# Performance work log

Hardware: AMD Instinct MI355X
Metric: run time of the kernel (lower is better)

Reference implementation:

```python
import jax, jax.numpy as jnp
import numpy as np

B, S, D, H, W1, G = 2, 4096, 768, 12, 256, 8  # W1 = one-sided window (attention_window // 2)
HD = D // H
NC = S // W1  # number of query chunks of size W1
NEG = -1e9


def setup_inputs():
    key = jax.random.key(0)
    ks = jax.random.split(key, 9)
    def w(k):
        return jax.random.normal(k, (D, D), jnp.float32) * 0.02
    zb = jnp.zeros((D,), jnp.float32)
    # mask: >0 global, 0 local, <0 masked. First G tokens are global.
    mask = jnp.zeros((B, 1, 1, S), jnp.int32).at[:, :, :, :G].set(1)
    return {
        "hidden_states": jax.random.normal(ks[0], (B, S, D), jnp.float32),
        "attention_mask": mask,
        "Wq": w(ks[1]), "bq": zb,
        "Wk": w(ks[2]), "bk": zb,
        "Wv": w(ks[3]), "bv": zb,
        "Wqg": w(ks[4]), "bqg": zb,
        "Wkg": w(ks[5]), "bkg": zb,
        "Wvg": w(ks[6]), "bvg": zb,
        "Wo": w(ks[7]), "bo": zb,
        "n_global": G,
    }


def reference(hidden_states, attention_mask, Wq, bq, Wk, bk, Wv, bv,
              Wqg, bqg, Wkg, bkg, Wvg, bvg, Wo, bo, n_global):
    g = n_global
    mask = attention_mask.reshape(B, S)
    key_neg = mask < 0  # masked-out positions
    scale = 1.0 / np.sqrt(HD)

    def heads(x):  # [B,S,D] -> [B,H,S,HD]
        return x.reshape(B, S, H, HD).transpose(0, 2, 1, 3)

    q = heads(hidden_states @ Wq + bq) * scale
    k = heads(hidden_states @ Wk + bk)
    v = heads(hidden_states @ Wv + bv)

    # ---- sliding-window (banded) scores via 3-chunk gather ----
    idx = jnp.arange(NC)[:, None] * W1 + jnp.arange(3 * W1)[None, :]  # [NC,3W] into padded seq
    k_ch = jnp.pad(k, ((0, 0), (0, 0), (W1, W1), (0, 0)))[:, :, idx]  # [B,H,NC,3W,HD]
    q_ch = q.reshape(B, H, NC, W1, HD)
    band = jnp.einsum('bhcqd,bhckd->bhcqk', q_ch, k_ch)  # [B,H,NC,W,3W]

    qi = jnp.arange(W1)
    kj = jnp.arange(3 * W1)
    band_ok = jnp.abs(kj[None, :] - W1 - qi[:, None]) <= W1        # [W,3W] |j-i|<=w
    j_abs = idx - W1                                               # absolute key index
    in_range = (j_abs >= 0) & (j_abs < S)                          # [NC,3W]
    neg_ch = jnp.pad(key_neg, ((0, 0), (W1, W1)))[:, idx]          # [B,NC,3W]
    valid = (band_ok[None, None, None]
             & in_range[None, None, :, None, :]
             & (~neg_ch)[:, None, :, None, :])                     # [B,1,NC,W,3W]
    band = jnp.where(valid, band, NEG)

    # ---- scores of every query against the global keys (regular k proj) ----
    glob = jnp.einsum('bhsd,bhgd->bhsg', q, k[:, :, :g])           # [B,H,S,G]
    glob = jnp.where(key_neg[:, None, None, :g], NEG, glob)

    scores = jnp.concatenate([glob.reshape(B, H, NC, W1, g), band], axis=-1)
    probs = jax.nn.softmax(scores, axis=-1)
    probs = jnp.where(key_neg.reshape(B, 1, NC, W1, 1), 0.0, probs)  # zero masked query rows

    v_ch = jnp.pad(v, ((0, 0), (0, 0), (W1, W1), (0, 0)))[:, :, idx]
    out = jnp.einsum('bhcqk,bhckd->bhcqd', probs[..., g:], v_ch)
    out = out + jnp.einsum('bhcqg,bhgd->bhcqd', probs[..., :g], v[:, :, :g])
    out = out.reshape(B, H, S, HD)

    # ---- global tokens: full attention with dedicated global projections ----
    qg = heads(hidden_states @ Wqg + bqg)[:, :, :g] * scale        # [B,H,G,HD]
    kg = heads(hidden_states @ Wkg + bkg)
    vg = heads(hidden_states @ Wvg + bvg)
    gs = jnp.einsum('bhgd,bhsd->bhgs', qg, kg)                     # [B,H,G,S]
    gs = jnp.where(key_neg[:, None, None, :], NEG, gs)
    gp = jax.nn.softmax(gs, axis=-1)
    og = jnp.einsum('bhgs,bhsd->bhgd', gp, vg)
    out = out.at[:, :, :g].set(og)

    merged = out.transpose(0, 2, 1, 3).reshape(B, S, D)
    return merged @ Wo + bo  # outer output projection
```

## Files before the change

kernel.cpp:

```cpp
#include <hip/hip_runtime.h>

#define BB 2
#define SS 4096
#define DD 768
#define HH 12
#define HDD 64
#define W1C 256
#define NCC 16
#define GG 8

typedef unsigned short u16;
typedef __attribute__((ext_vector_type(4))) unsigned short u16x4;
typedef __attribute__((ext_vector_type(8))) unsigned short u16x8;
typedef __attribute__((ext_vector_type(8))) short s16x8;
typedef __attribute__((ext_vector_type(4))) float f32x4;

__device__ __forceinline__ float b2f(u16 u) {
  union { unsigned int i; float f; } v;
  v.i = ((unsigned int)u) << 16;
  return v.f;
}
__device__ __forceinline__ u16 f2b(float f) {
  union { float f; unsigned int i; } v;
  v.f = f;
  unsigned int r = v.i + 0x7FFFu + ((v.i >> 16) & 1u);
  return (u16)(r >> 16);
}
__device__ __forceinline__ float fexp2(float x) {
#if __has_builtin(__builtin_amdgcn_exp2f)
  return __builtin_amdgcn_exp2f(x);
#else
  return exp2f(x);
#endif
}
__device__ __forceinline__ unsigned pk_bf16(float lo, float hi) {
  unsigned r;
  asm("v_cvt_pk_bf16_f32 %0, %1, %2" : "=v"(r) : "v"(lo), "v"(hi));
  return r;
}
__device__ __forceinline__ void load_lds16(const void* g, void* l) {
  __builtin_amdgcn_global_load_lds(
      (const __attribute__((address_space(1))) unsigned int*)g,
      (__attribute__((address_space(3))) unsigned int*)l, 16, 0, 0);
}

#define QSCALE 0.18033688011112042f

__global__ __launch_bounds__(256) void cvt_f32_bf16(
    const float* __restrict__ in, u16* __restrict__ out, int n8) {
  int i = blockIdx.x * 256 + threadIdx.x;
  if (i >= n8) return;
  const float4* p = (const float4*)(in + (size_t)i * 8);
  float4 a = p[0], b = p[1];
  u16x8 o;
  o[0] = f2b(a.x); o[1] = f2b(a.y); o[2] = f2b(a.z); o[3] = f2b(a.w);
  o[4] = f2b(b.x); o[5] = f2b(b.y); o[6] = f2b(b.z); o[7] = f2b(b.w);
  *(u16x8*)(out + (size_t)i * 8) = o;
}

struct WtArgs { const float* W[6]; };

__global__ __launch_bounds__(256) void transpose_wt(WtArgs wa,
                                                    u16* __restrict__ WT) {
  __shared__ float T[64][65];
  const int mat = blockIdx.z;
  const int k0 = blockIdx.y * 64;
  const int n0 = blockIdx.x * 64;
  const float* __restrict__ W = wa.W[mat];
  const int t = threadIdx.x;
#pragma unroll
  for (int i = 0; i < 4; i++) {
    int idx4 = t + i * 256;
    int r = idx4 >> 4, c4 = idx4 & 15;
    float4 v = *(const float4*)(W + (size_t)(k0 + r) * 768 + n0 + c4 * 4);
    T[r][c4 * 4 + 0] = v.x; T[r][c4 * 4 + 1] = v.y;
    T[r][c4 * 4 + 2] = v.z; T[r][c4 * 4 + 3] = v.w;
  }
  __syncthreads();
#pragma unroll
  for (int i = 0; i < 2; i++) {
    int ci = t + i * 256;
    int nl = ci >> 3, k8 = ci & 7;
    u16x8 o;
#pragma unroll
    for (int jj = 0; jj < 8; jj++) o[jj] = f2b(T[k8 * 8 + jj][nl]);
    *(u16x8*)(WT + ((size_t)mat * 768 + n0 + nl) * 768 + k0 + k8 * 8) = o;
  }
}

struct BiasArgs { const float* bias[5]; };

template <int MODE>
__global__ __launch_bounds__(256) void gemm_bf16(
    const u16* __restrict__ A, const u16* __restrict__ WT, BiasArgs ba,
    u16* __restrict__ outb, float* __restrict__ outf) {
  __shared__ __align__(16) u16 As[128 * 32];
  __shared__ __align__(16) u16 Bs[128 * 32];
  const int tid = threadIdx.x;
  const int w = tid >> 6, l = tid & 63;
  const int m0 = blockIdx.y * 128;
  const int wsel = (MODE == 0) ? ((int)blockIdx.x / 6) : 0;
  const int n0 =
      (MODE == 0) ? (((int)blockIdx.x % 6) * 128) : ((int)blockIdx.x * 128);
  const int nw0 = (int)blockIdx.x * 128;
  const float* __restrict__ bias = ba.bias[wsel];
  const int wm = w >> 1, wn = w & 1;
  const int srow = l >> 2;
  const int skc = (l & 3) * 8;

  f32x4 acc[4][4];
#pragma unroll
  for (int i = 0; i < 4; i++)
#pragma unroll
    for (int j = 0; j < 4; j++) acc[i][j] = (f32x4){0.f, 0.f, 0.f, 0.f};

  for (int k0 = 0; k0 < 768; k0 += 32) {
    __syncthreads();
#pragma unroll
    for (int i = 0; i < 2; i++) {
      const int ci = i * 4 + w;
      load_lds16(A + (size_t)(m0 + ci * 16 + srow) * 768 + k0 + skc,
                 (char*)As + ci * 1024);
    }
#pragma unroll
    for (int i = 0; i < 2; i++) {
      const int ci = i * 4 + w;
      load_lds16(WT + (size_t)(nw0 + ci * 16 + srow) * 768 + k0 + skc,
                 (char*)Bs + ci * 1024);
    }
    asm volatile("s_waitcnt vmcnt(0)" ::: "memory");
    __syncthreads();
    s16x8 af[4], bf[4];
#pragma unroll
    for (int mi = 0; mi < 4; mi++)
      af[mi] = *(const s16x8*)(As + (wm * 64 + mi * 16 + (l & 15)) * 32 +
                               (l >> 4) * 8);
#pragma unroll
    for (int nj = 0; nj < 4; nj++)
      bf[nj] = *(const s16x8*)(Bs + (wn * 64 + nj * 16 + (l & 15)) * 32 +
                               (l >> 4) * 8);
#pragma unroll
    for (int mi = 0; mi < 4; mi++)
#pragma unroll
      for (int nj = 0; nj < 4; nj++)
        acc[mi][nj] = __builtin_amdgcn_mfma_f32_16x16x32_bf16(
            af[mi], bf[nj], acc[mi][nj], 0, 0, 0);
  }

  const int rbase = (l >> 4) * 4;
  const int cl = l & 15;
  if (MODE == 0) {
    const float scale = (wsel == 0) ? QSCALE : 1.0f;
    u16* outw = outb + (size_t)wsel * ((size_t)BB * HH * SS * HDD);
#pragma unroll
    for (int nj = 0; nj < 4; nj++) {
      const int c = n0 + wn * 64 + nj * 16 + cl;
      const float bv = bias[c];
      const int h = c >> 6, hd = c & 63;
#pragma unroll
      for (int mi = 0; mi < 4; mi++) {
#pragma unroll
        for (int r = 0; r < 4; r++) {
          const int m = m0 + wm * 64 + mi * 16 + rbase + r;
          const int b = m >> 12, s = m & 4095;
          outw[((size_t)(b * HH + h) * SS + s) * HDD + hd] =
              f2b((acc[mi][nj][r] + bv) * scale);
        }
      }
    }
  } else {
#pragma unroll
    for (int nj = 0; nj < 4; nj++) {
      const int c = n0 + wn * 64 + nj * 16 + cl;
      const float bv = bias[c];
#pragma unroll
      for (int mi = 0; mi < 4; mi++) {
#pragma unroll
        for (int r = 0; r < 4; r++) {
          const int m = m0 + wm * 64 + mi * 16 + rbase + r;
          outf[(size_t)m * 768 + c] = acc[mi][nj][r] + bv;
        }
      }
    }
  }
}

__global__ __launch_bounds__(256) void qg_proj(
    const float* __restrict__ hs, const float* __restrict__ Wqg,
    const float* __restrict__ bqg, u16* __restrict__ QG) {
  __shared__ float hsL[8][768];
  const int bh = blockIdx.x;
  const int b = bh / HH, h = bh % HH;
  const int t = threadIdx.x;
#pragma unroll
  for (int i = 0; i < 6; i++) {
    int idx = t + i * 256;
    int row = idx / 192, c4 = idx % 192;
    *(float4*)&hsL[row][c4 * 4] =
        *(const float4*)(hs + ((size_t)b * SS + row) * DD + c4 * 4);
  }
  __syncthreads();
#pragma unroll
  for (int rep = 0; rep < 2; rep++) {
    int qi = rep * 4 + (t >> 6);
    int d = t & 63, n = h * 64 + d;
    float acc = bqg[n];
    for (int k = 0; k < DD; k++)
      acc = fmaf(hsL[qi][k], Wqg[(size_t)k * DD + n], acc);
    QG[((size_t)bh * 16 + qi) * 64 + d] = f2b(acc * QSCALE);
  }
#pragma unroll
  for (int i = 0; i < 2; i++) {
    int idx = t + i * 256;
    int row = 8 + (idx >> 6), d = idx & 63;
    QG[((size_t)bh * 16 + row) * 64 + d] = 0;
  }
}

template <int GLOBAL>
__global__ __launch_bounds__(256) void attn_mfma(
    const u16* __restrict__ Q, const u16* __restrict__ K,
    const u16* __restrict__ V, const int* __restrict__ amask,
    u16* __restrict__ ATT, float* __restrict__ Pnum,
    float* __restrict__ Pden) {
  extern __shared__ __align__(16) char smem[];
  const int tid = threadIdx.x;
  const int w = tid >> 6, lane = tid & 63;
  const int lq = lane & 15, g = lane >> 4;
  const int h = blockIdx.y, b = blockIdx.z;
  const int bh = b * HH + h;
  const size_t bhs = (size_t)bh * SS;
  const int q0 = GLOBAL ? 0 : (int)blockIdx.x * 64;
  const int split = GLOBAL ? (int)blockIdx.x : 0;

  char* Kl;
  char* VT;
  if constexpr (GLOBAL) {
    Kl = smem + w * 16384;
    VT = Kl + 8192;
  } else {
    Kl = smem;
    VT = smem + 8192;
  }

  s16x8 qf[2];
  {
    const u16* qp = GLOBAL ? (Q + ((size_t)bh * 16 + lq) * 64)
                           : (Q + (bhs + q0 + w * 16 + lq) * 64);
    qf[0] = *(const s16x8*)(qp + g * 8);
    qf[1] = *(const s16x8*)(qp + 32 + g * 8);
  }

  f32x4 oacc[4];
#pragma unroll
  for (int i = 0; i < 4; i++) oacc[i] = (f32x4){0.f, 0.f, 0.f, 0.f};
  float denom = 0.f;

  const int NT = GLOBAL ? 2 : 10;
  for (int kt = 0; kt < NT; kt++) {
    int j0, klimit;
    bool bandfree;
    if constexpr (GLOBAL) {
      j0 = split * 512 + (w * 2 + kt) * 64;
      bandfree = true;
      klimit = 64;
    } else {
      if (kt < 9) { j0 = q0 - 256 + kt * 64; bandfree = false; klimit = 64; }
      else        { j0 = 0;                  bandfree = true;  klimit = 8; }
    }

    int jm = j0 + lane;
    int mv = ((unsigned)jm < (unsigned)SS) ? amask[b * SS + jm] : -1;
    bool okk = (mv >= 0) && (lane < klimit);
    unsigned long long vm = __ballot(okk);

    if constexpr (GLOBAL) {
      asm volatile("s_waitcnt lgkmcnt(0)" ::: "memory");
      const u16* Ks = K + bhs * 64 + (size_t)j0 * 64;
#pragma unroll
      for (int i = 0; i < 8; i++) {
        int ci = i * 64 + lane;
        int row = ci >> 3, cc = ci & 7, cs = cc ^ (row & 7);
        load_lds16(Ks + row * 64 + cs * 8, Kl + i * 1024);
      }
      const u16* Vs = V + bhs * 64 + (size_t)j0 * 64;
#pragma unroll
      for (int p = 0; p < 8; p++) {
        u16x8 vv = *(const u16x8*)(Vs + (size_t)lane * 64 + p * 8);
#pragma unroll
        for (int e = 0; e < 8; e++)
          *(u16*)(VT + (p * 8 + e) * 128 + ((lane * 2) ^ (e << 4))) = vv[e];
      }
      asm volatile("s_waitcnt vmcnt(0) lgkmcnt(0)" ::: "memory");
    } else {
      __syncthreads();
      if (j0 >= 0 && j0 + 64 <= SS) {
        const u16* Ks = K + bhs * 64 + (size_t)j0 * 64;
#pragma unroll
        for (int i = 0; i < 2; i++) {
          int ci = (i * 4 + w) * 64 + lane;
          int row = ci >> 3, cc = ci & 7, cs = cc ^ (row & 7);
          load_lds16(Ks + row * 64 + cs * 8, Kl + (i * 4 + w) * 1024);
        }
      } else {
#pragma unroll
        for (int i = 0; i < 2; i++) {
          int ci = (i * 4 + w) * 64 + lane;
          int row = ci >> 3, cc = ci & 7, cs = cc ^ (row & 7);
          int jj = j0 + row;
          u16x8 val;
#pragma unroll
          for (int e = 0; e < 8; e++) val[e] = 0;
          if ((unsigned)jj < (unsigned)SS)
            val = *(const u16x8*)(K + (bhs + jj) * 64 + cs * 8);
          *(u16x8*)(Kl + ci * 16) = val;
        }
      }
#pragma unroll
      for (int p = 0; p < 2; p++) {
        int d0 = p * 32 + w * 8;
        int jj = j0 + lane;
        u16x8 vv;
#pragma unroll
        for (int e = 0; e < 8; e++) vv[e] = 0;
        if ((unsigned)jj < (unsigned)SS)
          vv = *(const u16x8*)(V + (bhs + jj) * 64 + d0);
#pragma unroll
        for (int e = 0; e < 8; e++)
          *(u16*)(VT + (d0 + e) * 128 + ((lane * 2) ^ (e << 4))) = vv[e];
      }
      asm volatile("s_waitcnt vmcnt(0)" ::: "memory");
      __syncthreads();
    }

    f32x4 sc[4];
#pragma unroll
    for (int i = 0; i < 4; i++) sc[i] = (f32x4){0.f, 0.f, 0.f, 0.f};
#pragma unroll
    for (int s = 0; s < 2; s++) {
#pragma unroll
      for (int ks = 0; ks < 4; ks++) {
        s16x8 kf = *(const s16x8*)(Kl + (ks * 16 + lq) * 128 +
                                   (((s * 4 + g) ^ (lq & 7)) << 4));
        sc[ks] = __builtin_amdgcn_mfma_f32_16x16x32_bf16(kf, qf[s], sc[ks],
                                                          0, 0, 0);
      }
    }

    {
      const unsigned mlo = (unsigned)vm, mhi = (unsigned)(vm >> 32);
      const int q_abs = q0 + w * 16 + lq;
      bool allin = bandfree;
      if constexpr (!GLOBAL) {
        const int qw = q0 + w * 16;
        allin = bandfree || (j0 >= qw - 241 && j0 <= qw + 193);
      }
      const bool fast = (vm == ~0ull) && allin;
      const int ddq = j0 + g * 4 - q_abs;
      const int gsh = g * 4;
      if (fast) {
#pragma unroll
        for (int ks = 0; ks < 4; ks++)
#pragma unroll
          for (int r = 0; r < 4; r++) {
            float p = fexp2(sc[ks][r]);
            sc[ks][r] = p;
            denom += p;
          }
      } else {
#pragma unroll
        for (int ks = 0; ks < 4; ks++)
#pragma unroll
          for (int r = 0; r < 4; r++) {
            float e = fexp2(sc[ks][r]);
            unsigned bit =
                ((ks < 2 ? mlo : mhi) >> (gsh + ((ks & 1) * 16 + r))) & 1u;
            bool ok = bit && (allin ||
                              (unsigned)(ddq + ks * 16 + r + 256) <= 512u);
            float p = ok ? e : 0.f;
            sc[ks][r] = p;
            denom += p;
          }
      }
    }

#pragma unroll
    for (int s = 0; s < 2; s++) {
      const int srcA = lq + ((g & 1) << 5);
      const bool hiSel = g >= 2;
      float L[4], H[4];
#pragma unroll
      for (int r = 0; r < 4; r++) {
        float a0 = __shfl(sc[2 * s][r], srcA);
        float a1 = __shfl(sc[2 * s + 1][r], srcA);
        L[r] = hiSel ? a1 : a0;
        float b0 = __shfl(sc[2 * s][r], srcA + 16);
        float b1 = __shfl(sc[2 * s + 1][r], srcA + 16);
        H[r] = hiSel ? b1 : b0;
      }
      union { unsigned u[4]; s16x8 v; } pf;
      pf.u[0] = pk_bf16(L[0], L[1]);
      pf.u[1] = pk_bf16(L[2], L[3]);
      pf.u[2] = pk_bf16(H[0], H[1]);
      pf.u[3] = pk_bf16(H[2], H[3]);
#pragma unroll
      for (int dblk = 0; dblk < 4; dblk++) {
        s16x8 vf = *(const s16x8*)(VT + (dblk * 16 + lq) * 128 +
                                   (((s * 4 + g) ^ (lq & 7)) << 4));
        oacc[dblk] = __builtin_amdgcn_mfma_f32_16x16x32_bf16(vf, pf.v,
                                                              oacc[dblk],
                                                              0, 0, 0);
      }
    }
  }

  denom += __shfl_xor(denom, 16);
  denom += __shfl_xor(denom, 32);
  if constexpr (!GLOBAL) {
    const int q_abs = q0 + w * 16 + lq;
    const float rowscale = (amask[b * SS + q_abs] >= 0) ? (1.f / denom) : 0.f;
    u16* orow = ATT + ((size_t)b * SS + q_abs) * DD + h * 64;
#pragma unroll
    for (int dblk = 0; dblk < 4; dblk++) {
      u16x4 o;
#pragma unroll
      for (int r = 0; r < 4; r++) o[r] = f2b(oacc[dblk][r] * rowscale);
      *(u16x4*)(orow + dblk * 16 + g * 4) = o;
    }
  } else {
    const int pidx = split * 4 + w;
    float* np = Pnum + ((size_t)bh * 32 + pidx) * 1024;
#pragma unroll
    for (int dblk = 0; dblk < 4; dblk++)
#pragma unroll
      for (int r = 0; r < 4; r++)
        np[(dblk * 16 + g * 4 + r) * 16 + lq] = oacc[dblk][r];
    Pden[((size_t)bh * 32 + pidx) * 16 + lq] = denom;
  }
}

__global__ __launch_bounds__(512) void gmerge(const float* __restrict__ Pnum,
                                              const float* __restrict__ Pden,
                                              u16* __restrict__ ATT) {
  const int bh = blockIdx.x;
  const int b = bh / HH, h = bh % HH;
  const int t = threadIdx.x;
  const int q = t >> 6, d = t & 63;
  float num = 0.f, den = 0.f;
#pragma unroll 4
  for (int p = 0; p < 32; p++) {
    num += Pnum[((size_t)bh * 32 + p) * 1024 + d * 16 + q];
    den += Pden[((size_t)bh * 32 + p) * 16 + q];
  }
  ATT[((size_t)b * SS + q) * DD + h * 64 + d] = f2b(num / den);
}

extern "C" void kernel_launch(void* const* d_in, const int* in_sizes, int n_in,
                              void* d_out, int out_size, void* d_ws,
                              size_t ws_size, hipStream_t stream) {
  const float* hs = (const float*)d_in[0];
  const int* amask = (const int*)d_in[1];
  const float* Wq = (const float*)d_in[2];
  const float* bq = (const float*)d_in[3];
  const float* Wk = (const float*)d_in[4];
  const float* bk = (const float*)d_in[5];
  const float* Wv = (const float*)d_in[6];
  const float* bv = (const float*)d_in[7];
  const float* Wqg = (const float*)d_in[8];
  const float* bqg = (const float*)d_in[9];
  const float* Wkg = (const float*)d_in[10];
  const float* bkg = (const float*)d_in[11];
  const float* Wvg = (const float*)d_in[12];
  const float* bvg = (const float*)d_in[13];
  const float* Wo = (const float*)d_in[14];
  const float* bo = (const float*)d_in[15];
  float* out = (float*)d_out;

  char* ws = (char*)d_ws;
  const size_t QSZB = (size_t)BB * HH * SS * HDD * 2;
  u16* Qb = (u16*)(ws + 0);
  u16* Kb = (u16*)(ws + QSZB);
  u16* Vb = (u16*)(ws + 2 * QSZB);
  u16* KGb = (u16*)(ws + 3 * QSZB);
  u16* VGb = (u16*)(ws + 4 * QSZB);
  u16* Ab = (u16*)(ws + 5 * QSZB);
  u16* WTb = (u16*)(ws + 6 * QSZB);
  u16* ATTb = (u16*)(ws + 6 * QSZB + 7077888);
  u16* QGb = (u16*)(ws + 7 * QSZB + 7077888);
  float* Pnum = (float*)(ws + 7 * QSZB + 7077888 + 49152);
  float* Pden = (float*)(ws + 7 * QSZB + 7077888 + 49152 + 3145728);

  hipLaunchKernelGGL(cvt_f32_bf16, dim3(3072), dim3(256), 0, stream, hs, Ab,
                     (int)((size_t)BB * SS * DD / 8));

  WtArgs wa;
  wa.W[0] = Wq; wa.W[1] = Wk; wa.W[2] = Wv;
  wa.W[3] = Wkg; wa.W[4] = Wvg; wa.W[5] = Wo;
  hipLaunchKernelGGL(transpose_wt, dim3(12, 12, 6), dim3(256), 0, stream, wa,
                     WTb);

  BiasArgs b0;
  b0.bias[0] = bq; b0.bias[1] = bk; b0.bias[2] = bv;
  b0.bias[3] = bkg; b0.bias[4] = bvg;
  hipLaunchKernelGGL((gemm_bf16<0>), dim3(30, 64), dim3(256), 0, stream, Ab,
                     WTb, b0, Qb, (float*)nullptr);

  hipLaunchKernelGGL(qg_proj, dim3(24), dim3(256), 0, stream, hs, Wqg, bqg,
                     QGb);

  hipLaunchKernelGGL((attn_mfma<1>), dim3(8, HH, BB), dim3(256), 65536,
                     stream, QGb, KGb, VGb, amask, (u16*)nullptr, Pnum, Pden);

  hipLaunchKernelGGL((attn_mfma<0>), dim3(64, HH, BB), dim3(256), 16384,
                     stream, Qb, Kb, Vb, amask, ATTb, (float*)nullptr,
                     (float*)nullptr);

  hipLaunchKernelGGL(gmerge, dim3(24), dim3(512), 0, stream, Pnum, Pden, ATTb);

  BiasArgs b1;
  for (int i = 0; i < 5; i++) b1.bias[i] = bo;
  hipLaunchKernelGGL((gemm_bf16<1>), dim3(6, 64), dim3(256), 0, stream, ATTb,
                     WTb + (size_t)5 * 768 * 768, b1, (u16*)nullptr, out);
}
```

Before: 213.2 us.

## Double GEMM K-tile, XOR-swizzle LDS layout, and XCD-aware block remap

The bf16 GEMM now stages K=64 per iteration instead of 32, which halves the number of barrier and global-wait rounds. Its LDS tiles use an XOR swizzle on the 16-byte chunk index to cut bank conflicts on the MFMA fragment reads. The grid is flattened to 1D and remapped so that consecutive tiles land on the same XCD (id&7 striping), aiming for better L2 reuse. LDS use doubles to 32KB per block, which may lower occupancy.

```diff
diff --git a/kernel.cpp b/kernel.cpp
--- a/kernel.cpp
+++ b/kernel.cpp
@@ -94,19 +94,25 @@
 __global__ __launch_bounds__(256) void gemm_bf16(
     const u16* __restrict__ A, const u16* __restrict__ WT, BiasArgs ba,
     u16* __restrict__ outb, float* __restrict__ outf) {
-  __shared__ __align__(16) u16 As[128 * 32];
-  __shared__ __align__(16) u16 Bs[128 * 32];
+  __shared__ __align__(16) u16 As[128 * 64];
+  __shared__ __align__(16) u16 Bs[128 * 64];
   const int tid = threadIdx.x;
   const int w = tid >> 6, l = tid & 63;
-  const int m0 = blockIdx.y * 128;
-  const int wsel = (MODE == 0) ? ((int)blockIdx.x / 6) : 0;
-  const int n0 =
-      (MODE == 0) ? (((int)blockIdx.x % 6) * 128) : ((int)blockIdx.x * 128);
-  const int nw0 = (int)blockIdx.x * 128;
+  const int lq = l & 15, g = l >> 4;
+
+  const int NB = (MODE == 0) ? 30 : 6;
+  const int nwg = NB * 64;
+  const int cpx = nwg >> 3;
+  const int id = (int)blockIdx.x;
+  const int swz = (id & 7) * cpx + (id >> 3);
+  const int bn = swz % NB, bm = swz / NB;
+
+  const int m0 = bm * 128;
+  const int wsel = (MODE == 0) ? (bn / 6) : 0;
+  const int n0 = (MODE == 0) ? ((bn % 6) * 128) : (bn * 128);
+  const int nw0 = bn * 128;
   const float* __restrict__ bias = ba.bias[wsel];
   const int wm = w >> 1, wn = w & 1;
-  const int srow = l >> 2;
-  const int skc = (l & 3) * 8;
 
   f32x4 acc[4][4];
 #pragma unroll
@@ -114,41 +120,50 @@
 #pragma unroll
     for (int j = 0; j < 4; j++) acc[i][j] = (f32x4){0.f, 0.f, 0.f, 0.f};
 
-  for (int k0 = 0; k0 < 768; k0 += 32) {
+  for (int k0 = 0; k0 < 768; k0 += 64) {
     __syncthreads();
 #pragma unroll
-    for (int i = 0; i < 2; i++) {
-      const int ci = i * 4 + w;
-      load_lds16(A + (size_t)(m0 + ci * 16 + srow) * 768 + k0 + skc,
-                 (char*)As + ci * 1024);
-    }
-#pragma unroll
-    for (int i = 0; i < 2; i++) {
-      const int ci = i * 4 + w;
-      load_lds16(WT + (size_t)(nw0 + ci * 16 + srow) * 768 + k0 + skc,
-                 (char*)Bs + ci * 1024);
+    for (int j = 0; j < 4; j++) {
+      const int ci = (j * 4 + w) * 64 + l;
+      const int row = ci >> 3, sl = ci & 7;
+      const int src = sl ^ (row & 7);
+      load_lds16(A + (size_t)(m0 + row) * 768 + k0 + src * 8,
+                 (char*)As + (j * 4 + w) * 1024);
+    }
+#pragma unroll
+    for (int j = 0; j < 4; j++) {
+      const int ci = (j * 4 + w) * 64 + l;
+      const int row = ci >> 3, sl = ci & 7;
+      const int src = sl ^ (row & 7);
+      load_lds16(WT + (size_t)(nw0 + row) * 768 + k0 + src * 8,
+                 (char*)Bs + (j * 4 + w) * 1024);
     }
     asm volatile("s_waitcnt vmcnt(0)" ::: "memory");
     __syncthreads();
-    s16x8 af[4], bf[4];
-#pragma unroll
-    for (int mi = 0; mi < 4; mi++)
-      af[mi] = *(const s16x8*)(As + (wm * 64 + mi * 16 + (l & 15)) * 32 +
-                               (l >> 4) * 8);
-#pragma unroll
-    for (int nj = 0; nj < 4; nj++)
-      bf[nj] = *(const s16x8*)(Bs + (wn * 64 + nj * 16 + (l & 15)) * 32 +
-                               (l >> 4) * 8);
-#pragma unroll
-    for (int mi = 0; mi < 4; mi++)
-#pragma unroll
-      for (int nj = 0; nj < 4; nj++)
-        acc[mi][nj] = __builtin_amdgcn_mfma_f32_16x16x32_bf16(
-            af[mi], bf[nj], acc[mi][nj], 0, 0, 0);
-  }
-
-  const int rbase = (l >> 4) * 4;
-  const int cl = l & 15;
+#pragma unroll
+    for (int s = 0; s < 2; s++) {
+      s16x8 af[4], bf[4];
+#pragma unroll
+      for (int mi = 0; mi < 4; mi++) {
+        const int r = wm * 64 + mi * 16 + lq;
+        af[mi] = *(const s16x8*)(As + r * 64 + (((s * 4 + g) ^ (r & 7)) * 8));
+      }
+#pragma unroll
+      for (int nj = 0; nj < 4; nj++) {
+        const int r = wn * 64 + nj * 16 + lq;
+        bf[nj] = *(const s16x8*)(Bs + r * 64 + (((s * 4 + g) ^ (r & 7)) * 8));
+      }
+#pragma unroll
+      for (int mi = 0; mi < 4; mi++)
+#pragma unroll
+        for (int nj = 0; nj < 4; nj++)
+          acc[mi][nj] = __builtin_amdgcn_mfma_f32_16x16x32_bf16(
+              af[mi], bf[nj], acc[mi][nj], 0, 0, 0);
+    }
+  }
+
+  const int rbase = g * 4;
+  const int cl = lq;
   if (MODE == 0) {
     const float scale = (wsel == 0) ? QSCALE : 1.0f;
     u16* outw = outb + (size_t)wsel * ((size_t)BB * HH * SS * HDD);
@@ -502,7 +517,7 @@
   BiasArgs b0;
   b0.bias[0] = bq; b0.bias[1] = bk; b0.bias[2] = bv;
   b0.bias[3] = bkg; b0.bias[4] = bvg;
-  hipLaunchKernelGGL((gemm_bf16<0>), dim3(30, 64), dim3(256), 0, stream, Ab,
+  hipLaunchKernelGGL((gemm_bf16<0>), dim3(1920), dim3(256), 0, stream, Ab,
                      WTb, b0, Qb, (float*)nullptr);
 
   hipLaunchKernelGGL(qg_proj, dim3(24), dim3(256), 0, stream, hs, Wqg, bqg,
@@ -519,6 +534,6 @@
 
   BiasArgs b1;
   for (int i = 0; i < 5; i++) b1.bias[i] = bo;
-  hipLaunchKernelGGL((gemm_bf16<1>), dim3(6, 64), dim3(256), 0, stream, ATTb,
+  hipLaunchKernelGGL((gemm_bf16<1>), dim3(384), dim3(256), 0, stream, ATTb,
                      WTb + (size_t)5 * 768 * 768, b1, (u16*)nullptr, out);
 }
```

Result: faster. 208.9 us (-2.0%).
